# Kernel tuning notes

Hardware: AMD Instinct MI355X
Metric: run time of the kernel (lower is better)

The kernel has to match this reference:

```python
import jax, jax.numpy as jnp
import numpy as np

NUM_HEADS = 6

def setup_inputs() -> dict:
    key = jax.random.key(0)
    k1, k2, k3, k4 = jax.random.split(key, 4)
    B, T, C = 128, 256, 384
    s = 1.0 / np.sqrt(C)
    return {
        'x': jax.random.normal(k1, (B, T, C), dtype=jnp.float32),
        'Wq': jax.random.normal(k2, (C, C), dtype=jnp.float32) * s,
        'Wk': jax.random.normal(k3, (C, C), dtype=jnp.float32) * s,
        'Wv': jax.random.normal(k4, (C, C), dtype=jnp.float32) * s,
    }

def reference(x, Wq, Wk, Wv):
    B, T, C = x.shape
    H = NUM_HEADS
    d = C // H
    # projections (bias-free Linear), split into heads
    q = (x @ Wq).reshape(B, T, H, d)
    k = (x @ Wk).reshape(B, T, H, d)
    v = (x @ Wv).reshape(B, T, H, d)
    # NOTE: original scales by 1/sqrt(C), not 1/sqrt(head_dim)
    scale = 1.0 / jnp.sqrt(jnp.asarray(C, dtype=x.dtype))
    att = jnp.einsum('bqhd,bkhd->bhqk', q, k) * scale  # [B,H,T,T]
    causal = jnp.tril(jnp.ones((T, T), dtype=bool))
    att = jnp.where(causal, att, -jnp.inf)
    att = jax.nn.softmax(att, axis=-1)
    # dropout is identity in eval/deterministic mode
    out = jnp.einsum('bhqk,bkhd->bqhd', att, v)  # [B,T,H,d]
    return out.reshape(B, T, C)
```

## Files before the change

kernel.cpp:

```cpp
#include <hip/hip_runtime.h>


typedef unsigned short u16;
typedef float f32x4 __attribute__((ext_vector_type(4)));
typedef short s16x8 __attribute__((ext_vector_type(8)));
typedef u16 u16x4 __attribute__((ext_vector_type(4)));

static constexpr int BB = 128;
static constexpr int TT = 256;
static constexpr int CC = 384;
static constexpr int HH = 6;
static constexpr int DD = 64;
static constexpr int MM = BB * TT;

static constexpr size_t WTOFF = 0;
static constexpr size_t XOFF  = (size_t)3 * CC * CC;

static constexpr float CSC = 0.07362242194579907f;

__device__ __forceinline__ u16 f2bf(float f) {
  unsigned u = __float_as_uint(f);
  u += 0x7fffu + ((u >> 16) & 1u);
  return (u16)(u >> 16);
}

__device__ __forceinline__ void g2l16(const u16* g, u16* l) {
  __builtin_amdgcn_global_load_lds(
      (const __attribute__((address_space(1))) u16*)g,
      (__attribute__((address_space(3))) u16*)l, 16, 0, 0);
}

__global__ void prep(const float* __restrict__ X, const float* __restrict__ Wq,
                     const float* __restrict__ Wk, const float* __restrict__ Wv,
                     u16* __restrict__ ws) {
  int bx = blockIdx.x;
  if (bx < 6144) {
    size_t i = (size_t)(bx * 256 + threadIdx.x) * 8;
    f32x4 a0 = *(const f32x4*)(X + i);
    f32x4 a1 = *(const f32x4*)(X + i + 4);
    s16x8 ab;
#pragma unroll
    for (int j = 0; j < 4; ++j) { ab[j] = (short)f2bf(a0[j]); ab[4 + j] = (short)f2bf(a1[j]); }
    *(s16x8*)(ws + XOFF + i) = ab;
  } else {
    __shared__ u16 Lt[64][66];
    int j = bx - 6144;
    int z = j / 36, t = j % 36, ti = t / 6, tj = t % 6;
    const float* W = (z == 0) ? Wq : (z == 1) ? Wk : Wv;
    const float sc = (z == 0) ? CSC : 1.0f;
    u16* WT = ws + WTOFF + (size_t)z * CC * CC;
    const int rl = threadIdx.x >> 4;
    const int cl = (threadIdx.x & 15) * 4;
#pragma unroll
    for (int it = 0; it < 4; ++it) {
      int r = it * 16 + rl;
      f32x4 v = *(const f32x4*)(W + (size_t)(ti * 64 + r) * CC + tj * 64 + cl);
#pragma unroll
      for (int q = 0; q < 4; ++q) Lt[r][cl + q] = f2bf(v[q] * sc);
    }
    __syncthreads();
#pragma unroll
    for (int it = 0; it < 4; ++it) {
      int n = it * 16 + rl;
      u16x4 o;
#pragma unroll
      for (int q = 0; q < 4; ++q) o[q] = Lt[cl + q][n];
      *(u16x4*)(WT + (size_t)(tj * 64 + n) * CC + ti * 64 + cl) = o;
    }
  }
}

__global__ __launch_bounds__(1024, 4) void fused(const u16* __restrict__ ws,
                                                 float* __restrict__ out) {
  const int bid = blockIdx.x;
  const int xc = bid & 7;
  const int g5 = bid >> 3;
  const int b = xc * 16 + g5 / 6;
  const int h = g5 % 6;

  __shared__ u16 R1[256][64];
  __shared__ u16 R2[16][1152];
  __shared__ u16 Ks[256][64];
  __shared__ u16 VTs[64][256];

  const int tid = threadIdx.x;
  const int lane = tid & 63;
  const int w = tid >> 6;
  const int quad = lane >> 4;
  const int col = lane & 15;
  const int a = w >> 2;
  const int bq = w & 3;
  const int wm = a * 64;
  const int wn = bq * 48;

  const u16* Xg = ws + XOFF + (size_t)b * TT * CC;
  const u16* Wg = ws + WTOFF;
  u16* Wst = &R2[0][0];

  const int rl = lane >> 3;
  const int gb = (lane & 7) ^ rl;

  auto stage = [&](int kt) {
    int r0 = w * 16;
    g2l16(Xg + (size_t)(r0 + rl) * CC + kt * 64 + gb * 8, &R1[r0][0]);
    g2l16(Xg + (size_t)(r0 + 8 + rl) * CC + kt * 64 + gb * 8, &R1[r0 + 8][0]);
    {
      int rr = w * 8 + rl;
      int z = rr >> 6, nn = rr & 63;
      g2l16(Wg + (size_t)(z * CC + h * DD + nn) * CC + kt * 64 + gb * 8,
            Wst + w * 512);
    }
    if (w < 8) {
      int c = w + 16;
      int rr = c * 8 + rl;
      int z = rr >> 6, nn = rr & 63;
      g2l16(Wg + (size_t)(z * CC + h * DD + nn) * CC + kt * 64 + gb * 8,
            Wst + c * 512);
    }
  };

  f32x4 acc[4][3] = {};

  stage(0);
  asm volatile("s_waitcnt vmcnt(0)" ::: "memory");
  __syncthreads();

  for (int kt = 0; kt < 6; ++kt) {
    s16x8 af[4][2], bf[3][2];
#pragma unroll
    for (int mt = 0; mt < 4; ++mt)
#pragma unroll
      for (int ks = 0; ks < 2; ++ks)
        af[mt][ks] = *(const s16x8*)(&R1[wm + mt * 16 + col]
                                        [(((ks * 4 + quad) ^ (col & 7)) * 8)]);
#pragma unroll
    for (int nt = 0; nt < 3; ++nt)
#pragma unroll
      for (int ks = 0; ks < 2; ++ks)
        bf[nt][ks] = *(const s16x8*)(Wst + (wn + nt * 16 + col) * 64 +
                                     (((ks * 4 + quad) ^ (col & 7)) * 8));

    __syncthreads();
    if (kt < 5) stage(kt + 1);

#pragma unroll
    for (int ks = 0; ks < 2; ++ks)
#pragma unroll
      for (int mt = 0; mt < 4; ++mt)
#pragma unroll
        for (int nt = 0; nt < 3; ++nt)
          acc[mt][nt] = __builtin_amdgcn_mfma_f32_16x16x32_bf16(
              af[mt][ks], bf[nt][ks], acc[mt][nt], 0, 0, 0);

    if (kt < 5) {
      asm volatile("s_waitcnt vmcnt(0)" ::: "memory");
      __syncthreads();
    }
  }

#pragma unroll
  for (int mt = 0; mt < 4; ++mt) {
    int tokb = wm + mt * 16 + quad * 4;
#pragma unroll
    for (int nt = 0; nt < 3; ++nt) {
      int gn = wn + nt * 16 + col;
      if (gn < 128) {
        u16* dst = (gn < 64) ? &R1[0][0] : &Ks[0][0];
        int d = gn & 63;
#pragma unroll
        for (int r = 0; r < 4; ++r) {
          int tok = tokb + r;
          dst[tok * 64 + (d ^ ((tok & 7) << 3))] = f2bf(acc[mt][nt][r]);
        }
      } else {
        int d = gn - 128;
        uint2 pk;
        pk.x = (unsigned)f2bf(acc[mt][nt][0]) | ((unsigned)f2bf(acc[mt][nt][1]) << 16);
        pk.y = (unsigned)f2bf(acc[mt][nt][2]) | ((unsigned)f2bf(acc[mt][nt][3]) << 16);
        *(uint2*)((u16*)VTs + d * 256 + (tokb ^ ((d & 15) << 3))) = pk;
      }
    }
  }
  __syncthreads();

  const int gcl = (a + bq) & 3;
  const int g = gcl * 4 + a;
  const int kthi = g >> 2;
  const int qq = (g & 3) * 16 + col;
  u16* Ps = &R2[w][col * 72];

  s16x8 qf[2];
  {
    int q = g * 16 + col;
#pragma unroll
    for (int ks = 0; ks < 2; ++ks)
      qf[ks] = *(const s16x8*)(&R1[q][(((ks * 4 + quad) ^ (q & 7)) * 8)]);
  }

  f32x4 o[4] = {};
  float mst = -1.0e30f, lst = 0.0f;

  for (int kt = 0; kt <= kthi; ++kt) {
    s16x8 kf[4][2], vf[4][2];
#pragma unroll
    for (int nt = 0; nt < 4; ++nt)
#pragma unroll
      for (int ks = 0; ks < 2; ++ks) {
        int key = kt * 64 + nt * 16 + col;
        kf[nt][ks] = *(const s16x8*)(&Ks[key][(((ks * 4 + quad) ^ (col & 7)) * 8)]);
        int d = nt * 16 + col;
        vf[nt][ks] = *(const s16x8*)((const u16*)VTs + d * 256 +
                     ((kt * 64 + ks * 32 + quad * 8) ^ ((d & 15) << 3)));
      }

    f32x4 s[4] = {};
#pragma unroll
    for (int ks = 0; ks < 2; ++ks)
#pragma unroll
      for (int nt = 0; nt < 4; ++nt)
        s[nt] = __builtin_amdgcn_mfma_f32_16x16x32_bf16(kf[nt][ks], qf[ks],
                                                        s[nt], 0, 0, 0);

    const bool diag = (kt == kthi);
    float rmax = -1.0e30f;
#pragma unroll
    for (int nt = 0; nt < 4; ++nt)
#pragma unroll
      for (int r = 0; r < 4; ++r) {
        float t = s[nt][r];
        if (diag && (nt * 16 + quad * 4 + r) > qq) t = -1.0e30f;
        s[nt][r] = t;
        rmax = fmaxf(rmax, t);
      }
    rmax = fmaxf(rmax, __shfl_xor(rmax, 16));
    rmax = fmaxf(rmax, __shfl_xor(rmax, 32));

    float mn = fmaxf(mst, rmax);
    float alpha = exp2f(mst - mn);
    mst = mn;

    float lsum = 0.0f;
    unsigned pk[4][2];
#pragma unroll
    for (int nt = 0; nt < 4; ++nt) {
      float p0 = exp2f(s[nt][0] - mn), p1 = exp2f(s[nt][1] - mn);
      float p2 = exp2f(s[nt][2] - mn), p3 = exp2f(s[nt][3] - mn);
      lsum += (p0 + p1) + (p2 + p3);
      pk[nt][0] = (unsigned)f2bf(p0) | ((unsigned)f2bf(p1) << 16);
      pk[nt][1] = (unsigned)f2bf(p2) | ((unsigned)f2bf(p3) << 16);
    }
    lst = lst * alpha + lsum;

    asm volatile("s_waitcnt lgkmcnt(0)" ::: "memory");
#pragma unroll
    for (int nt = 0; nt < 4; ++nt)
      *(uint2*)(Ps + nt * 16 + quad * 4) = make_uint2(pk[nt][0], pk[nt][1]);

#pragma unroll
    for (int dt = 0; dt < 4; ++dt)
#pragma unroll
      for (int r = 0; r < 4; ++r) o[dt][r] *= alpha;

    asm volatile("s_waitcnt lgkmcnt(0)" ::: "memory");
    s16x8 pf[2];
#pragma unroll
    for (int ks = 0; ks < 2; ++ks)
      pf[ks] = *(const s16x8*)(Ps + ks * 32 + quad * 8);

#pragma unroll
    for (int ks = 0; ks < 2; ++ks)
#pragma unroll
      for (int dt = 0; dt < 4; ++dt)
        o[dt] = __builtin_amdgcn_mfma_f32_16x16x32_bf16(vf[dt][ks], pf[ks],
                                                        o[dt], 0, 0, 0);
  }

  {
    float l = lst;
    l += __shfl_xor(l, 16);
    l += __shfl_xor(l, 32);
    float inv = 1.0f / l;
    int q = g * 16 + col;
#pragma unroll
    for (int dt = 0; dt < 4; ++dt) {
      f32x4 res;
#pragma unroll
      for (int r = 0; r < 4; ++r) res[r] = o[dt][r] * inv;
      *(f32x4*)(out + (size_t)(b * TT + q) * CC + h * DD + dt * 16 + quad * 4) = res;
    }
  }
}

extern "C" void kernel_launch(void* const* d_in, const int* in_sizes, int n_in,
                              void* d_out, int out_size, void* d_ws, size_t ws_size,
                              hipStream_t stream) {
  const float* x  = (const float*)d_in[0];
  const float* wq = (const float*)d_in[1];
  const float* wk = (const float*)d_in[2];
  const float* wv = (const float*)d_in[3];
  u16* ws  = (u16*)d_ws;
  float* out = (float*)d_out;

  prep<<<dim3(6144 + 108), 256, 0, stream>>>(x, wq, wk, wv, ws);
  fused<<<dim3(BB * HH), 1024, 0, stream>>>(ws, out);
}
```

Baseline: 167.2 us.

## Halve fused block to 8 waves with balanced causal query-tile pairing

The fused kernel now runs with 512 threads instead of 1024. In the projection GEMM each wave computes a wider 64x96 tile, and the staging loops are adjusted to match. In the attention phase each wave handles two query tiles, g and 15-g, so the causal work is balanced across waves, and the shared K/V fragment loads are reused for both tiles. It also adds s_setprio around the MFMA blocks, XOR-swizzles the P scratch buffer, and drops the explicit vmcnt waits before barriers. In exchange it raises register pressure and lowers thread-level parallelism per block.

```diff
diff --git a/kernel.cpp b/kernel.cpp
--- a/kernel.cpp
+++ b/kernel.cpp
@@ -70,8 +70,8 @@
   }
 }
 
-__global__ __launch_bounds__(1024, 4) void fused(const u16* __restrict__ ws,
-                                                 float* __restrict__ out) {
+__global__ __launch_bounds__(512, 2) void fused(const u16* __restrict__ ws,
+                                                float* __restrict__ out) {
   const int bid = blockIdx.x;
   const int xc = bid & 7;
   const int g5 = bid >> 3;
@@ -79,7 +79,7 @@
   const int h = g5 % 6;
 
   __shared__ u16 R1[256][64];
-  __shared__ u16 R2[16][1152];
+  __shared__ u16 R2[16384];
   __shared__ u16 Ks[256][64];
   __shared__ u16 VTs[64][256];
 
@@ -88,45 +88,40 @@
   const int w = tid >> 6;
   const int quad = lane >> 4;
   const int col = lane & 15;
-  const int a = w >> 2;
-  const int bq = w & 3;
-  const int wm = a * 64;
-  const int wn = bq * 48;
 
   const u16* Xg = ws + XOFF + (size_t)b * TT * CC;
   const u16* Wg = ws + WTOFF;
-  u16* Wst = &R2[0][0];
+  u16* Wst = R2;
 
   const int rl = lane >> 3;
   const int gb = (lane & 7) ^ rl;
 
+  const int wm = (w >> 1) * 64;
+  const int wn = (w & 1) * 96;
+
   auto stage = [&](int kt) {
-    int r0 = w * 16;
-    g2l16(Xg + (size_t)(r0 + rl) * CC + kt * 64 + gb * 8, &R1[r0][0]);
-    g2l16(Xg + (size_t)(r0 + 8 + rl) * CC + kt * 64 + gb * 8, &R1[r0 + 8][0]);
-    {
-      int rr = w * 8 + rl;
+#pragma unroll
+    for (int i = 0; i < 4; ++i) {
+      int r0 = w * 32 + i * 8;
+      g2l16(Xg + (size_t)(r0 + rl) * CC + kt * 64 + gb * 8, &R1[r0][0]);
+    }
+#pragma unroll
+    for (int i = 0; i < 3; ++i) {
+      int r0 = w * 24 + i * 8;
+      int rr = r0 + rl;
       int z = rr >> 6, nn = rr & 63;
       g2l16(Wg + (size_t)(z * CC + h * DD + nn) * CC + kt * 64 + gb * 8,
-            Wst + w * 512);
-    }
-    if (w < 8) {
-      int c = w + 16;
-      int rr = c * 8 + rl;
-      int z = rr >> 6, nn = rr & 63;
-      g2l16(Wg + (size_t)(z * CC + h * DD + nn) * CC + kt * 64 + gb * 8,
-            Wst + c * 512);
+            Wst + r0 * 64);
     }
   };
 
-  f32x4 acc[4][3] = {};
+  f32x4 acc[4][6] = {};
 
   stage(0);
-  asm volatile("s_waitcnt vmcnt(0)" ::: "memory");
   __syncthreads();
 
   for (int kt = 0; kt < 6; ++kt) {
-    s16x8 af[4][2], bf[3][2];
+    s16x8 af[4][2], bf[6][2];
 #pragma unroll
     for (int mt = 0; mt < 4; ++mt)
 #pragma unroll
@@ -134,7 +129,7 @@
         af[mt][ks] = *(const s16x8*)(&R1[wm + mt * 16 + col]
                                         [(((ks * 4 + quad) ^ (col & 7)) * 8)]);
 #pragma unroll
-    for (int nt = 0; nt < 3; ++nt)
+    for (int nt = 0; nt < 6; ++nt)
 #pragma unroll
       for (int ks = 0; ks < 2; ++ks)
         bf[nt][ks] = *(const s16x8*)(Wst + (wn + nt * 16 + col) * 64 +
@@ -143,26 +138,25 @@
     __syncthreads();
     if (kt < 5) stage(kt + 1);
 
+    __builtin_amdgcn_s_setprio(1);
 #pragma unroll
     for (int ks = 0; ks < 2; ++ks)
 #pragma unroll
       for (int mt = 0; mt < 4; ++mt)
 #pragma unroll
-        for (int nt = 0; nt < 3; ++nt)
+        for (int nt = 0; nt < 6; ++nt)
           acc[mt][nt] = __builtin_amdgcn_mfma_f32_16x16x32_bf16(
               af[mt][ks], bf[nt][ks], acc[mt][nt], 0, 0, 0);
-
-    if (kt < 5) {
-      asm volatile("s_waitcnt vmcnt(0)" ::: "memory");
-      __syncthreads();
-    }
+    __builtin_amdgcn_s_setprio(0);
+
+    if (kt < 5) __syncthreads();
   }
 
 #pragma unroll
   for (int mt = 0; mt < 4; ++mt) {
     int tokb = wm + mt * 16 + quad * 4;
 #pragma unroll
-    for (int nt = 0; nt < 3; ++nt) {
+    for (int nt = 0; nt < 6; ++nt) {
       int gn = wn + nt * 16 + col;
       if (gn < 128) {
         u16* dst = (gn < 64) ? &R1[0][0] : &Ks[0][0];
@@ -183,45 +177,28 @@
   }
   __syncthreads();
 
-  const int gcl = (a + bq) & 3;
-  const int g = gcl * 4 + a;
-  const int kthi = g >> 2;
-  const int qq = (g & 3) * 16 + col;
-  u16* Ps = &R2[w][col * 72];
-
-  s16x8 qf[2];
+  const int g0 = w, g1 = 15 - w;
+  const int k0max = g0 >> 2, k1max = g1 >> 2;
+  const int qq0 = (g0 & 3) * 16 + col;
+  const int qq1 = (g1 & 3) * 16 + col;
+  u16* PsA = R2 + w * 2048;
+  u16* PsB = PsA + 1024;
+
+  s16x8 qf[2][2];
   {
-    int q = g * 16 + col;
-#pragma unroll
-    for (int ks = 0; ks < 2; ++ks)
-      qf[ks] = *(const s16x8*)(&R1[q][(((ks * 4 + quad) ^ (q & 7)) * 8)]);
-  }
-
-  f32x4 o[4] = {};
-  float mst = -1.0e30f, lst = 0.0f;
-
-  for (int kt = 0; kt <= kthi; ++kt) {
-    s16x8 kf[4][2], vf[4][2];
-#pragma unroll
-    for (int nt = 0; nt < 4; ++nt)
-#pragma unroll
-      for (int ks = 0; ks < 2; ++ks) {
-        int key = kt * 64 + nt * 16 + col;
-        kf[nt][ks] = *(const s16x8*)(&Ks[key][(((ks * 4 + quad) ^ (col & 7)) * 8)]);
-        int d = nt * 16 + col;
-        vf[nt][ks] = *(const s16x8*)((const u16*)VTs + d * 256 +
-                     ((kt * 64 + ks * 32 + quad * 8) ^ ((d & 15) << 3)));
-      }
-
-    f32x4 s[4] = {};
-#pragma unroll
-    for (int ks = 0; ks < 2; ++ks)
-#pragma unroll
-      for (int nt = 0; nt < 4; ++nt)
-        s[nt] = __builtin_amdgcn_mfma_f32_16x16x32_bf16(kf[nt][ks], qf[ks],
-                                                        s[nt], 0, 0, 0);
-
-    const bool diag = (kt == kthi);
+    int qr0 = g0 * 16 + col, qr1 = g1 * 16 + col;
+#pragma unroll
+    for (int ks = 0; ks < 2; ++ks) {
+      qf[0][ks] = *(const s16x8*)(&R1[qr0][(((ks * 4 + quad) ^ (col & 7)) * 8)]);
+      qf[1][ks] = *(const s16x8*)(&R1[qr1][(((ks * 4 + quad) ^ (col & 7)) * 8)]);
+    }
+  }
+
+  f32x4 o[2][4] = {};
+  float mst[2] = {-1.0e30f, -1.0e30f}, lst[2] = {0.0f, 0.0f};
+
+  auto sm = [&](f32x4 (&s)[4], bool diag, int qq, float& m, float& l,
+                unsigned (&pk)[4][2]) -> float {
     float rmax = -1.0e30f;
 #pragma unroll
     for (int nt = 0; nt < 4; ++nt)
@@ -234,13 +211,10 @@
       }
     rmax = fmaxf(rmax, __shfl_xor(rmax, 16));
     rmax = fmaxf(rmax, __shfl_xor(rmax, 32));
-
-    float mn = fmaxf(mst, rmax);
-    float alpha = exp2f(mst - mn);
-    mst = mn;
-
+    float mn = fmaxf(m, rmax);
+    float alpha = exp2f(m - mn);
+    m = mn;
     float lsum = 0.0f;
-    unsigned pk[4][2];
 #pragma unroll
     for (int nt = 0; nt < 4; ++nt) {
       float p0 = exp2f(s[nt][0] - mn), p1 = exp2f(s[nt][1] - mn);
@@ -249,34 +223,105 @@
       pk[nt][0] = (unsigned)f2bf(p0) | ((unsigned)f2bf(p1) << 16);
       pk[nt][1] = (unsigned)f2bf(p2) | ((unsigned)f2bf(p3) << 16);
     }
-    lst = lst * alpha + lsum;
+    l = l * alpha + lsum;
+    return alpha;
+  };
+
+  for (int kt = 0; kt <= k1max; ++kt) {
+    const bool both = (kt <= k0max);
+
+    s16x8 kf[4][2], vf[4][2];
+#pragma unroll
+    for (int nt = 0; nt < 4; ++nt)
+#pragma unroll
+      for (int ks = 0; ks < 2; ++ks) {
+        int key = kt * 64 + nt * 16 + col;
+        kf[nt][ks] = *(const s16x8*)(&Ks[key][(((ks * 4 + quad) ^ (col & 7)) * 8)]);
+        int d = nt * 16 + col;
+        vf[nt][ks] = *(const s16x8*)((const u16*)VTs + d * 256 +
+                     ((kt * 64 + ks * 32 + quad * 8) ^ ((d & 15) << 3)));
+      }
+
+    f32x4 sA[4] = {}, sB[4] = {};
+    __builtin_amdgcn_s_setprio(1);
+    if (both) {
+#pragma unroll
+      for (int ks = 0; ks < 2; ++ks)
+#pragma unroll
+        for (int nt = 0; nt < 4; ++nt)
+          sA[nt] = __builtin_amdgcn_mfma_f32_16x16x32_bf16(kf[nt][ks], qf[0][ks],
+                                                           sA[nt], 0, 0, 0);
+    }
+#pragma unroll
+    for (int ks = 0; ks < 2; ++ks)
+#pragma unroll
+      for (int nt = 0; nt < 4; ++nt)
+        sB[nt] = __builtin_amdgcn_mfma_f32_16x16x32_bf16(kf[nt][ks], qf[1][ks],
+                                                         sB[nt], 0, 0, 0);
+    __builtin_amdgcn_s_setprio(0);
+
+    unsigned pkA[4][2], pkB[4][2];
+    float aA = 1.0f, aB;
+    if (both) {
+      aA = sm(sA, kt == k0max, qq0, mst[0], lst[0], pkA);
+#pragma unroll
+      for (int nt = 0; nt < 4; ++nt)
+        *(uint2*)(PsA + col * 64 + ((nt * 16 + quad * 4) ^ ((col & 7) << 3))) =
+            make_uint2(pkA[nt][0], pkA[nt][1]);
+    }
+    aB = sm(sB, kt == k1max, qq1, mst[1], lst[1], pkB);
+#pragma unroll
+    for (int nt = 0; nt < 4; ++nt)
+      *(uint2*)(PsB + col * 64 + ((nt * 16 + quad * 4) ^ ((col & 7) << 3))) =
+          make_uint2(pkB[nt][0], pkB[nt][1]);
+
+    if (both) {
+#pragma unroll
+      for (int dt = 0; dt < 4; ++dt)
+#pragma unroll
+        for (int r = 0; r < 4; ++r) o[0][dt][r] *= aA;
+    }
+#pragma unroll
+    for (int dt = 0; dt < 4; ++dt)
+#pragma unroll
+      for (int r = 0; r < 4; ++r) o[1][dt][r] *= aB;
 
     asm volatile("s_waitcnt lgkmcnt(0)" ::: "memory");
-#pragma unroll
-    for (int nt = 0; nt < 4; ++nt)
-      *(uint2*)(Ps + nt * 16 + quad * 4) = make_uint2(pk[nt][0], pk[nt][1]);
-
-#pragma unroll
-    for (int dt = 0; dt < 4; ++dt)
-#pragma unroll
-      for (int r = 0; r < 4; ++r) o[dt][r] *= alpha;
-
-    asm volatile("s_waitcnt lgkmcnt(0)" ::: "memory");
-    s16x8 pf[2];
+
+    s16x8 pfA[2], pfB[2];
+    if (both) {
+#pragma unroll
+      for (int ks = 0; ks < 2; ++ks)
+        pfA[ks] = *(const s16x8*)(PsA + col * 64 +
+                                  ((ks * 32 + quad * 8) ^ ((col & 7) << 3)));
+    }
 #pragma unroll
     for (int ks = 0; ks < 2; ++ks)
-      pf[ks] = *(const s16x8*)(Ps + ks * 32 + quad * 8);
-
+      pfB[ks] = *(const s16x8*)(PsB + col * 64 +
+                                ((ks * 32 + quad * 8) ^ ((col & 7) << 3)));
+
+    __builtin_amdgcn_s_setprio(1);
+    if (both) {
+#pragma unroll
+      for (int ks = 0; ks < 2; ++ks)
+#pragma unroll
+        for (int dt = 0; dt < 4; ++dt)
+          o[0][dt] = __builtin_amdgcn_mfma_f32_16x16x32_bf16(vf[dt][ks], pfA[ks],
+                                                             o[0][dt], 0, 0, 0);
+    }
 #pragma unroll
     for (int ks = 0; ks < 2; ++ks)
 #pragma unroll
       for (int dt = 0; dt < 4; ++dt)
-        o[dt] = __builtin_amdgcn_mfma_f32_16x16x32_bf16(vf[dt][ks], pf[ks],
-                                                        o[dt], 0, 0, 0);
-  }
-
-  {
-    float l = lst;
+        o[1][dt] = __builtin_amdgcn_mfma_f32_16x16x32_bf16(vf[dt][ks], pfB[ks],
+                                                           o[1][dt], 0, 0, 0);
+    __builtin_amdgcn_s_setprio(0);
+  }
+
+#pragma unroll
+  for (int gi = 0; gi < 2; ++gi) {
+    int g = gi ? g1 : g0;
+    float l = lst[gi];
     l += __shfl_xor(l, 16);
     l += __shfl_xor(l, 32);
     float inv = 1.0f / l;
@@ -285,7 +330,7 @@
     for (int dt = 0; dt < 4; ++dt) {
       f32x4 res;
 #pragma unroll
-      for (int r = 0; r < 4; ++r) res[r] = o[dt][r] * inv;
+      for (int r = 0; r < 4; ++r) res[r] = o[gi][dt][r] * inv;
       *(f32x4*)(out + (size_t)(b * TT + q) * CC + h * DD + dt * 16 + quad * 4) = res;
     }
   }
@@ -302,5 +347,5 @@
   float* out = (float*)d_out;
 
   prep<<<dim3(6144 + 108), 256, 0, stream>>>(x, wq, wk, wv, ws);
-  fused<<<dim3(BB * HH), 1024, 0, stream>>>(ws, out);
-}
+  fused<<<dim3(BB * HH), 512, 0, stream>>>(ws, out);
+}
```

Result: faster. 154.9 us (-7.4%).
